# Performance work log

Hardware: AMD Instinct MI355X
Metric: run time of the kernel (lower is better)

Reference implementation:

```python
import jax, jax.numpy as jnp
import numpy as np

T, B = 100, 512
DIMS = [700, 512, 20]
ALPHA = 0.8   # 1 - dt/tau_s = 1 - 0.001/0.005
BETA = 0.9    # 1 - dt/tau_m = 1 - 0.001/0.010
THR = 1.0     # snntorch default threshold


@jax.custom_vjp
def spike(x):
    # Heaviside with ATan surrogate gradient (snntorch default, alpha=2)
    return (x > 0).astype(x.dtype)

def _spike_fwd(x):
    return spike(x), x

def _spike_bwd(x, g):
    # d/dx atan surrogate with alpha=2: 1 / (1 + (pi*x)^2)
    return (g / (1.0 + (jnp.pi * x) ** 2),)

spike.defvjp(_spike_fwd, _spike_bwd)


def setup_inputs() -> dict:
    key = jax.random.key(0)
    kx, k1, k2 = jax.random.split(key, 3)
    x = jax.random.uniform(kx, (T, B, DIMS[0]), dtype=jnp.float32)
    # kaiming_normal_ on weight [d2, d1]: std = sqrt(2 / fan_in), fan_in = d1
    W1 = jax.random.normal(k1, (DIMS[1], DIMS[0]), dtype=jnp.float32) * np.sqrt(2.0 / DIMS[0])
    W2 = jax.random.normal(k2, (DIMS[2], DIMS[1]), dtype=jnp.float32) * np.sqrt(2.0 / DIMS[1])
    return {"x": x, "W1": W1, "W2": W2}


def _spiking_linear(x, W):
    # x: [T, B, d_in], W: [d_out, d_in]
    pre = jnp.einsum('tbi,oi->tbo', x, W)  # per-timestep F.linear, batched over T

    def step(carry, p):
        syn, mem = carry
        syn = ALPHA * syn + p
        # reset from previous-step membrane, detached (snntorch mem_reset)
        reset = jax.lax.stop_gradient((mem > THR).astype(p.dtype))
        mem = (BETA * mem + syn) * (1.0 - reset)  # reset_mechanism='zero'
        spk = spike(mem - THR)
        return (syn, mem), spk

    z = jnp.zeros(pre.shape[1:], dtype=pre.dtype)
    _, spks = jax.lax.scan(step, (z, z), pre)
    return spks  # [T, B, d_out]


def reference(x, W1, W2):
    x = x.astype(jnp.float32)
    s1 = _spiking_linear(x, W1)
    s2 = _spiking_linear(s1, W2)
    # SNN2.forward returns (out, all_spikes=[layer1_spikes, layer2_spikes])
    return (s2, s1, s2)
```

## Files before the change

### kernel.cpp

```cpp
#include <hip/hip_runtime.h>

#define T_STEPS 100
#define BATCH   512
#define D0      700
#define D1      512
#define D2      20
#define M_ROWS  (T_STEPS * BATCH)

#define OFF_S2A 0
#define OFF_S1  (T_STEPS * BATCH * D2)
#define OFF_S2B (OFF_S1 + T_STEPS * BATCH * D1)

__device__ __constant__ const float kALPHA = 0.8f;
__device__ __constant__ const float kBETA  = 0.9f;
__device__ __constant__ const float kTHR   = 1.0f;

constexpr int BM = 128, BN = 128, BK = 32;

__device__ __forceinline__ int swz(int k, int m) {
    const int c = m >> 2;
    const int cpos = c ^ ((c >> 3) & 3) ^ ((k >> 2) & 7);
    return k * BM + (cpos << 2) + (m & 3);
}

__global__ __launch_bounds__(256)
void gemm1_kernel(const float* __restrict__ A, const float* __restrict__ W,
                  float* __restrict__ C) {
    __shared__ float As[BK * BM];
    __shared__ float Ws[BK * BN];

    const int d     = blockIdx.x;
    const int xcd   = d & 7;
    const int local = d >> 3;
    const int brow  = xcd * 50 + (local >> 2);
    const int bcol  = local & 3;

    const int tid  = threadIdx.x;
    const int row0 = brow * BM;
    const int col0 = bcol * BN;

    const int tx = tid & 15;
    const int ty = tid >> 4;

    const int ca0 = (2 * ty)     ^ (((2 * ty)     >> 3) & 3);
    const int ca1 = (2 * ty + 1) ^ (((2 * ty + 1) >> 3) & 3);
    const int cb0 = (2 * tx)     ^ (((2 * tx)     >> 3) & 3);
    const int cb1 = (2 * tx + 1) ^ (((2 * tx + 1) >> 3) & 3);

    float acc[8][8];
#pragma unroll
    for (int i = 0; i < 8; ++i)
#pragma unroll
        for (int j = 0; j < 8; ++j) acc[i][j] = 0.f;

    const int NT = (D0 + BK - 1) / BK;
    for (int kt = 0; kt < NT; ++kt) {
        const int k0 = kt * BK;
#pragma unroll
        for (int l = 0; l < 4; ++l) {
            const int f  = tid + l * 256;
            const int r  = f >> 3;
            const int c4 = f & 7;
            const int k  = c4 * 4;
            const int gk = k0 + k;

            float4 v, w;
            if (gk + 3 < D0) {
                v = *(const float4*)(A + (size_t)(row0 + r) * D0 + gk);
                w = *(const float4*)(W + (size_t)(col0 + r) * D0 + gk);
            } else {
                const float* ap = A + (size_t)(row0 + r) * D0;
                const float* wp = W + (size_t)(col0 + r) * D0;
                v.x = (gk + 0 < D0) ? ap[gk + 0] : 0.f;
                v.y = (gk + 1 < D0) ? ap[gk + 1] : 0.f;
                v.z = (gk + 2 < D0) ? ap[gk + 2] : 0.f;
                v.w = (gk + 3 < D0) ? ap[gk + 3] : 0.f;
                w.x = (gk + 0 < D0) ? wp[gk + 0] : 0.f;
                w.y = (gk + 1 < D0) ? wp[gk + 1] : 0.f;
                w.z = (gk + 2 < D0) ? wp[gk + 2] : 0.f;
                w.w = (gk + 3 < D0) ? wp[gk + 3] : 0.f;
            }
            As[swz(k + 0, r)] = v.x; As[swz(k + 1, r)] = v.y;
            As[swz(k + 2, r)] = v.z; As[swz(k + 3, r)] = v.w;
            Ws[swz(k + 0, r)] = w.x; Ws[swz(k + 1, r)] = w.y;
            Ws[swz(k + 2, r)] = w.z; Ws[swz(k + 3, r)] = w.w;
        }
        __syncthreads();

#pragma unroll
        for (int k = 0; k < BK; ++k) {
            const int kx = (k >> 2) & 7;
            const int kb = k * BM;
            float a[8], b[8];
            *(float4*)&a[0] = *(const float4*)&As[kb + ((ca0 ^ kx) << 2)];
            *(float4*)&a[4] = *(const float4*)&As[kb + ((ca1 ^ kx) << 2)];
            *(float4*)&b[0] = *(const float4*)&Ws[kb + ((cb0 ^ kx) << 2)];
            *(float4*)&b[4] = *(const float4*)&Ws[kb + ((cb1 ^ kx) << 2)];
#pragma unroll
            for (int i = 0; i < 8; ++i)
#pragma unroll
                for (int j = 0; j < 8; ++j)
                    acc[i][j] = fmaf(a[i], b[j], acc[i][j]);
        }
        __syncthreads();
    }

#pragma unroll
    for (int i = 0; i < 8; ++i) {
        float* cp = C + (size_t)(row0 + ty * 8 + i) * D1 + col0 + tx * 8;
        float4 v0 = make_float4(acc[i][0], acc[i][1], acc[i][2], acc[i][3]);
        float4 v1 = make_float4(acc[i][4], acc[i][5], acc[i][6], acc[i][7]);
        *(float4*)(cp + 0) = v0;
        *(float4*)(cp + 4) = v1;
    }
}

__global__ __launch_bounds__(256)
void scan1_kernel(float* __restrict__ buf) {
#pragma clang fp contract(off)
    const int idx = blockIdx.x * blockDim.x + threadIdx.x;
    const int stride = BATCH * D1;
    float syn = 0.f, mem = 0.f;
    float* p = buf + idx;
    for (int t = 0; t < T_STEPS; ++t) {
        const float pre = p[(size_t)t * stride];
        float a = kALPHA * syn;
        syn = a + pre;
        const float reset = (mem > kTHR) ? 1.f : 0.f;
        float bm = kBETA * mem;
        mem = (bm + syn) * (1.f - reset);
        p[(size_t)t * stride] = (mem > kTHR) ? 1.f : 0.f;
    }
}

__global__ __launch_bounds__(256)
void gemm2_kernel(const float* __restrict__ S1, const float* __restrict__ W2,
                  float* __restrict__ C) {
    __shared__ float Wsh[D2 * D1];
    for (int i = threadIdx.x; i < (D2 * D1) / 4; i += 256)
        ((float4*)Wsh)[i] = ((const float4*)W2)[i];
    __syncthreads();

    const int r  = threadIdx.x >> 2;
    const int kq = threadIdx.x & 3;
    const int m  = blockIdx.x * 64 + r;

    const float4* src = (const float4*)(S1 + (size_t)m * D1 + kq * 128);
    float acc[D2];
#pragma unroll
    for (int o = 0; o < D2; ++o) acc[o] = 0.f;

    for (int j = 0; j < 32; ++j) {
        const float4 v = src[j];
        const float* wbase = Wsh + kq * 128 + j * 4;
#pragma unroll
        for (int o = 0; o < D2; ++o) {
            const float4 w = *(const float4*)(wbase + o * D1);
            acc[o] += v.x * w.x + v.y * w.y + v.z * w.z + v.w * w.w;
        }
    }
#pragma unroll
    for (int o = 0; o < D2; ++o) {
        acc[o] += __shfl_xor(acc[o], 1);
        acc[o] += __shfl_xor(acc[o], 2);
    }
    if (kq == 0) {
        float* cp = C + (size_t)m * D2;
#pragma unroll
        for (int o = 0; o < D2; o += 4)
            *(float4*)(cp + o) = make_float4(acc[o], acc[o + 1], acc[o + 2], acc[o + 3]);
    }
}

__global__ __launch_bounds__(256)
void scan2_kernel(float* __restrict__ buf, float* __restrict__ dup) {
#pragma clang fp contract(off)
    const int idx = blockIdx.x * blockDim.x + threadIdx.x;
    const int stride = BATCH * D2;
    float syn = 0.f, mem = 0.f;
    for (int t = 0; t < T_STEPS; ++t) {
        const size_t off = (size_t)t * stride + idx;
        const float pre = buf[off];
        float a = kALPHA * syn;
        syn = a + pre;
        const float reset = (mem > kTHR) ? 1.f : 0.f;
        float bm = kBETA * mem;
        mem = (bm + syn) * (1.f - reset);
        const float s = (mem > kTHR) ? 1.f : 0.f;
        buf[off] = s;
        dup[off] = s;
    }
}

extern "C" void kernel_launch(void* const* d_in, const int* in_sizes, int n_in,
                              void* d_out, int out_size, void* d_ws, size_t ws_size,
                              hipStream_t stream) {
    const float* x  = (const float*)d_in[0];
    const float* W1 = (const float*)d_in[1];
    const float* W2 = (const float*)d_in[2];
    float* out = (float*)d_out;

    float* s2a = out + OFF_S2A;
    float* s1  = out + OFF_S1;
    float* s2b = out + OFF_S2B;

    gemm1_kernel<<<(M_ROWS / BM) * (D1 / BN), 256, 0, stream>>>(x, W1, s1);

    scan1_kernel<<<(BATCH * D1) / 256, 256, 0, stream>>>(s1);

    gemm2_kernel<<<M_ROWS / 64, 256, 0, stream>>>(s1, W2, s2a);

    scan2_kernel<<<(BATCH * D2) / 256, 256, 0, stream>>>(s2a, s2b);
}
```

Measured before the change: 608.5 us.

## Use 128 threads with 16x8 per-thread tile in first GEMM

Halves the block of the 700->512 GEMM to 128 threads and doubles each thread's output tile to 16x8, so each shared-memory fragment load feeds more FMAs. Global loads for the whole K tile are now gathered into registers before the shared-memory stores, which lets the loads overlap. The larger accumulator array (128 floats) and the staging registers raise register pressure and may lower occupancy or cause spills.

```diff
diff --git a/kernel.cpp b/kernel.cpp
--- a/kernel.cpp
+++ b/kernel.cpp
@@ -23,7 +23,7 @@
     return k * BM + (cpos << 2) + (m & 3);
 }
 
-__global__ __launch_bounds__(256)
+__global__ __launch_bounds__(128)
 void gemm1_kernel(const float* __restrict__ A, const float* __restrict__ W,
                   float* __restrict__ C) {
     __shared__ float As[BK * BM];
@@ -42,72 +42,85 @@
     const int tx = tid & 15;
     const int ty = tid >> 4;
 
-    const int ca0 = (2 * ty)     ^ (((2 * ty)     >> 3) & 3);
-    const int ca1 = (2 * ty + 1) ^ (((2 * ty + 1) >> 3) & 3);
+    int ca[4];
+#pragma unroll
+    for (int dd = 0; dd < 4; ++dd) {
+        const int u = 4 * ty + dd;
+        ca[dd] = u ^ ((u >> 3) & 3);
+    }
     const int cb0 = (2 * tx)     ^ (((2 * tx)     >> 3) & 3);
     const int cb1 = (2 * tx + 1) ^ (((2 * tx + 1) >> 3) & 3);
 
-    float acc[8][8];
-#pragma unroll
-    for (int i = 0; i < 8; ++i)
+    float acc[16][8];
+#pragma unroll
+    for (int i = 0; i < 16; ++i)
 #pragma unroll
         for (int j = 0; j < 8; ++j) acc[i][j] = 0.f;
 
     const int NT = (D0 + BK - 1) / BK;
     for (int kt = 0; kt < NT; ++kt) {
         const int k0 = kt * BK;
-#pragma unroll
-        for (int l = 0; l < 4; ++l) {
-            const int f  = tid + l * 256;
+        float4 va[8], vw[8];
+#pragma unroll
+        for (int l = 0; l < 8; ++l) {
+            const int f  = tid + l * 128;
             const int r  = f >> 3;
-            const int c4 = f & 7;
-            const int k  = c4 * 4;
+            const int k  = (f & 7) * 4;
             const int gk = k0 + k;
-
-            float4 v, w;
             if (gk + 3 < D0) {
-                v = *(const float4*)(A + (size_t)(row0 + r) * D0 + gk);
-                w = *(const float4*)(W + (size_t)(col0 + r) * D0 + gk);
+                va[l] = *(const float4*)(A + (size_t)(row0 + r) * D0 + gk);
+                vw[l] = *(const float4*)(W + (size_t)(col0 + r) * D0 + gk);
             } else {
                 const float* ap = A + (size_t)(row0 + r) * D0;
                 const float* wp = W + (size_t)(col0 + r) * D0;
-                v.x = (gk + 0 < D0) ? ap[gk + 0] : 0.f;
-                v.y = (gk + 1 < D0) ? ap[gk + 1] : 0.f;
-                v.z = (gk + 2 < D0) ? ap[gk + 2] : 0.f;
-                v.w = (gk + 3 < D0) ? ap[gk + 3] : 0.f;
-                w.x = (gk + 0 < D0) ? wp[gk + 0] : 0.f;
-                w.y = (gk + 1 < D0) ? wp[gk + 1] : 0.f;
-                w.z = (gk + 2 < D0) ? wp[gk + 2] : 0.f;
-                w.w = (gk + 3 < D0) ? wp[gk + 3] : 0.f;
+                va[l].x = (gk + 0 < D0) ? ap[gk + 0] : 0.f;
+                va[l].y = (gk + 1 < D0) ? ap[gk + 1] : 0.f;
+                va[l].z = (gk + 2 < D0) ? ap[gk + 2] : 0.f;
+                va[l].w = (gk + 3 < D0) ? ap[gk + 3] : 0.f;
+                vw[l].x = (gk + 0 < D0) ? wp[gk + 0] : 0.f;
+                vw[l].y = (gk + 1 < D0) ? wp[gk + 1] : 0.f;
+                vw[l].z = (gk + 2 < D0) ? wp[gk + 2] : 0.f;
+                vw[l].w = (gk + 3 < D0) ? wp[gk + 3] : 0.f;
             }
-            As[swz(k + 0, r)] = v.x; As[swz(k + 1, r)] = v.y;
-            As[swz(k + 2, r)] = v.z; As[swz(k + 3, r)] = v.w;
-            Ws[swz(k + 0, r)] = w.x; Ws[swz(k + 1, r)] = w.y;
-            Ws[swz(k + 2, r)] = w.z; Ws[swz(k + 3, r)] = w.w;
+        }
+#pragma unroll
+        for (int l = 0; l < 8; ++l) {
+            const int f = tid + l * 128;
+            const int r = f >> 3;
+            const int k = (f & 7) * 4;
+            As[swz(k + 0, r)] = va[l].x; As[swz(k + 1, r)] = va[l].y;
+            As[swz(k + 2, r)] = va[l].z; As[swz(k + 3, r)] = va[l].w;
+            Ws[swz(k + 0, r)] = vw[l].x; Ws[swz(k + 1, r)] = vw[l].y;
+            Ws[swz(k + 2, r)] = vw[l].z; Ws[swz(k + 3, r)] = vw[l].w;
         }
         __syncthreads();
 
-#pragma unroll
-        for (int k = 0; k < BK; ++k) {
-            const int kx = (k >> 2) & 7;
-            const int kb = k * BM;
-            float a[8], b[8];
-            *(float4*)&a[0] = *(const float4*)&As[kb + ((ca0 ^ kx) << 2)];
-            *(float4*)&a[4] = *(const float4*)&As[kb + ((ca1 ^ kx) << 2)];
-            *(float4*)&b[0] = *(const float4*)&Ws[kb + ((cb0 ^ kx) << 2)];
-            *(float4*)&b[4] = *(const float4*)&Ws[kb + ((cb1 ^ kx) << 2)];
-#pragma unroll
-            for (int i = 0; i < 8; ++i)
-#pragma unroll
-                for (int j = 0; j < 8; ++j)
-                    acc[i][j] = fmaf(a[i], b[j], acc[i][j]);
+#pragma unroll 2
+        for (int kq = 0; kq < 8; ++kq) {
+#pragma unroll
+            for (int kk = 0; kk < 4; ++kk) {
+                const int k  = kq * 4 + kk;
+                const int kb = k * BM;
+                float a[16], b[8];
+                *(float4*)&a[0]  = *(const float4*)&As[kb + ((ca[0] ^ kq) << 2)];
+                *(float4*)&a[4]  = *(const float4*)&As[kb + ((ca[1] ^ kq) << 2)];
+                *(float4*)&a[8]  = *(const float4*)&As[kb + ((ca[2] ^ kq) << 2)];
+                *(float4*)&a[12] = *(const float4*)&As[kb + ((ca[3] ^ kq) << 2)];
+                *(float4*)&b[0]  = *(const float4*)&Ws[kb + ((cb0  ^ kq) << 2)];
+                *(float4*)&b[4]  = *(const float4*)&Ws[kb + ((cb1  ^ kq) << 2)];
+#pragma unroll
+                for (int i = 0; i < 16; ++i)
+#pragma unroll
+                    for (int j = 0; j < 8; ++j)
+                        acc[i][j] = fmaf(a[i], b[j], acc[i][j]);
+            }
         }
         __syncthreads();
     }
 
 #pragma unroll
-    for (int i = 0; i < 8; ++i) {
-        float* cp = C + (size_t)(row0 + ty * 8 + i) * D1 + col0 + tx * 8;
+    for (int i = 0; i < 16; ++i) {
+        float* cp = C + (size_t)(row0 + ty * 16 + i) * D1 + col0 + tx * 8;
         float4 v0 = make_float4(acc[i][0], acc[i][1], acc[i][2], acc[i][3]);
         float4 v1 = make_float4(acc[i][4], acc[i][5], acc[i][6], acc[i][7]);
         *(float4*)(cp + 0) = v0;
@@ -204,7 +217,7 @@
     float* s1  = out + OFF_S1;
     float* s2b = out + OFF_S2B;
 
-    gemm1_kernel<<<(M_ROWS / BM) * (D1 / BN), 256, 0, stream>>>(x, W1, s1);
+    gemm1_kernel<<<(M_ROWS / BM) * (D1 / BN), 128, 0, stream>>>(x, W1, s1);
 
     scan1_kernel<<<(BATCH * D1) / 256, 256, 0, stream>>>(s1);
 
```

Result: slower. 734.8 us (+20.8%).

## Double-buffer GEMM1 tiles with direct global-to-LDS async loads

Applied to the files above, without the earlier changes.

Rewrites the first GEMM's main loop to use two shared-memory buffers and stage the next K tile with global_load_lds (direct global-to-LDS DMA) while computing on the current one. The shared layout changes from k-major swizzled to row-major with an XOR swizzle on 16-byte chunks, read as float2 pairs. The last partial K tile is handled by clamping addresses and running only 14 of 16 k-pairs. This removes the per-tile register round trip and one barrier per iteration, and lets loads overlap the FMA work. In exchange it doubles LDS use, which may lower occupancy, and the clamped-address trick for the K tail is subtle to get right.

```diff
diff --git a/kernel.cpp b/kernel.cpp
--- a/kernel.cpp
+++ b/kernel.cpp
@@ -16,18 +16,68 @@
 __device__ __constant__ const float kTHR   = 1.0f;
 
 constexpr int BM = 128, BN = 128, BK = 32;
-
-__device__ __forceinline__ int swz(int k, int m) {
-    const int c = m >> 2;
-    const int cpos = c ^ ((c >> 3) & 3) ^ ((k >> 2) & 7);
-    return k * BM + (cpos << 2) + (m & 3);
+constexpr int TILE_F = BM * BK;
+
+#define HAS_GLL (__has_builtin(__builtin_amdgcn_global_load_lds))
+
+__device__ __forceinline__ void stage_tile(const float* __restrict__ gbase,
+                                           int row0, int kt, float* lbuf,
+                                           int wave, int lane) {
+#pragma unroll
+    for (int s = 0; s < 4; ++s) {
+        const int rloc = wave * 32 + s * 8;
+        const int gws  = (wave * 4 + s) & 7;
+        int koff = kt * 128 + (((lane & 7) ^ gws) << 4);
+        koff = koff > 2784 ? 2784 : koff;
+        const float* g = (const float*)((const char*)gbase
+                         + (size_t)(row0 + rloc + (lane >> 3)) * 2800 + koff);
+        float* l = lbuf + rloc * 32;
+#if HAS_GLL
+        __builtin_amdgcn_global_load_lds(
+            (const __attribute__((address_space(1))) void*)g,
+            (__attribute__((address_space(3))) void*)l, 16, 0, 0);
+#else
+        float4 v = *(const float4*)g;
+        *(float4*)&l[lane * 4] = v;
+#endif
+    }
+}
+
+template <int NP>
+__device__ __forceinline__ void compute_tile(const float* __restrict__ As,
+                                             const float* __restrict__ Ws,
+                                             int ty, int tx,
+                                             float acc[8][8]) {
+    const int tyg = ty & 7, txg = tx & 7;
+#pragma unroll
+    for (int p = 0; p < NP; ++p) {
+        const int c = p >> 1;
+        const int e = (p & 1) << 1;
+        float2 av[8], bv[8];
+#pragma unroll
+        for (int i = 0; i < 8; ++i)
+            av[i] = *(const float2*)&As[(ty * 8 + i) * 32 + ((c ^ tyg) << 2) + e];
+#pragma unroll
+        for (int j = 0; j < 8; ++j)
+            bv[j] = *(const float2*)&Ws[(tx * 8 + j) * 32 + ((c ^ txg) << 2) + e];
+#pragma unroll
+        for (int i = 0; i < 8; ++i)
+#pragma unroll
+            for (int j = 0; j < 8; ++j)
+                acc[i][j] = fmaf(av[i].x, bv[j].x, acc[i][j]);
+#pragma unroll
+        for (int i = 0; i < 8; ++i)
+#pragma unroll
+            for (int j = 0; j < 8; ++j)
+                acc[i][j] = fmaf(av[i].y, bv[j].y, acc[i][j]);
+    }
 }
 
 __global__ __launch_bounds__(256)
 void gemm1_kernel(const float* __restrict__ A, const float* __restrict__ W,
                   float* __restrict__ C) {
-    __shared__ float As[BK * BM];
-    __shared__ float Ws[BK * BN];
+    __shared__ float As[2][TILE_F];
+    __shared__ float Ws[2][TILE_F];
 
     const int d     = blockIdx.x;
     const int xcd   = d & 7;
@@ -38,14 +88,10 @@
     const int tid  = threadIdx.x;
     const int row0 = brow * BM;
     const int col0 = bcol * BN;
-
-    const int tx = tid & 15;
-    const int ty = tid >> 4;
-
-    const int ca0 = (2 * ty)     ^ (((2 * ty)     >> 3) & 3);
-    const int ca1 = (2 * ty + 1) ^ (((2 * ty + 1) >> 3) & 3);
-    const int cb0 = (2 * tx)     ^ (((2 * tx)     >> 3) & 3);
-    const int cb1 = (2 * tx + 1) ^ (((2 * tx + 1) >> 3) & 3);
+    const int wave = tid >> 6;
+    const int lane = tid & 63;
+    const int tx   = tid & 15;
+    const int ty   = tid >> 4;
 
     float acc[8][8];
 #pragma unroll
@@ -53,56 +99,24 @@
 #pragma unroll
         for (int j = 0; j < 8; ++j) acc[i][j] = 0.f;
 
-    const int NT = (D0 + BK - 1) / BK;
+    const int NT = 22;
+
+    stage_tile(A, row0, 0, As[0], wave, lane);
+    stage_tile(W, col0, 0, Ws[0], wave, lane);
+    __syncthreads();
+
+    int buf = 0;
     for (int kt = 0; kt < NT; ++kt) {
-        const int k0 = kt * BK;
-#pragma unroll
-        for (int l = 0; l < 4; ++l) {
-            const int f  = tid + l * 256;
-            const int r  = f >> 3;
-            const int c4 = f & 7;
-            const int k  = c4 * 4;
-            const int gk = k0 + k;
-
-            float4 v, w;
-            if (gk + 3 < D0) {
-                v = *(const float4*)(A + (size_t)(row0 + r) * D0 + gk);
-                w = *(const float4*)(W + (size_t)(col0 + r) * D0 + gk);
-            } else {
-                const float* ap = A + (size_t)(row0 + r) * D0;
-                const float* wp = W + (size_t)(col0 + r) * D0;
-                v.x = (gk + 0 < D0) ? ap[gk + 0] : 0.f;
-                v.y = (gk + 1 < D0) ? ap[gk + 1] : 0.f;
-                v.z = (gk + 2 < D0) ? ap[gk + 2] : 0.f;
-                v.w = (gk + 3 < D0) ? ap[gk + 3] : 0.f;
-                w.x = (gk + 0 < D0) ? wp[gk + 0] : 0.f;
-                w.y = (gk + 1 < D0) ? wp[gk + 1] : 0.f;
-                w.z = (gk + 2 < D0) ? wp[gk + 2] : 0.f;
-                w.w = (gk + 3 < D0) ? wp[gk + 3] : 0.f;
-            }
-            As[swz(k + 0, r)] = v.x; As[swz(k + 1, r)] = v.y;
-            As[swz(k + 2, r)] = v.z; As[swz(k + 3, r)] = v.w;
-            Ws[swz(k + 0, r)] = w.x; Ws[swz(k + 1, r)] = w.y;
-            Ws[swz(k + 2, r)] = w.z; Ws[swz(k + 3, r)] = w.w;
+        if (kt + 1 < NT) {
+            stage_tile(A, row0, kt + 1, As[buf ^ 1], wave, lane);
+            stage_tile(W, col0, kt + 1, Ws[buf ^ 1], wave, lane);
         }
+        if (kt + 1 < NT)
+            compute_tile<16>(As[buf], Ws[buf], ty, tx, acc);
+        else
+            compute_tile<14>(As[buf], Ws[buf], ty, tx, acc);
         __syncthreads();
-
-#pragma unroll
-        for (int k = 0; k < BK; ++k) {
-            const int kx = (k >> 2) & 7;
-            const int kb = k * BM;
-            float a[8], b[8];
-            *(float4*)&a[0] = *(const float4*)&As[kb + ((ca0 ^ kx) << 2)];
-            *(float4*)&a[4] = *(const float4*)&As[kb + ((ca1 ^ kx) << 2)];
-            *(float4*)&b[0] = *(const float4*)&Ws[kb + ((cb0 ^ kx) << 2)];
-            *(float4*)&b[4] = *(const float4*)&Ws[kb + ((cb1 ^ kx) << 2)];
-#pragma unroll
-            for (int i = 0; i < 8; ++i)
-#pragma unroll
-                for (int j = 0; j < 8; ++j)
-                    acc[i][j] = fmaf(a[i], b[j], acc[i][j]);
-        }
-        __syncthreads();
+        buf ^= 1;
     }
 
 #pragma unroll
```

Measured after the change: 809.4 us. +33.0%, slower.
